# Performance work log

Measured on AMD Instinct MI355X. Metric: run time of the kernel, lower is better.

Reference implementation:

```python
import jax, jax.numpy as jnp
import numpy as np

N, T, D, H = 8192, 60, 6, 64  # stocks, lookback, d_feat, hidden_size
NEG_SLOPE = 0.01


def setup_inputs() -> dict:
    key = jax.random.key(0)
    ks = jax.random.split(key, 16)
    s = 0.1
    inp = {
        "x": jax.random.normal(ks[0], (N, D * T), jnp.float32),
        # GRU layer 0 (input D -> H), PyTorch gate order [r, z, n]
        "gru_Wih0": jax.random.normal(ks[1], (3 * H, D), jnp.float32) * s,
        "gru_Whh0": jax.random.normal(ks[2], (3 * H, H), jnp.float32) * s,
        "gru_bih0": jax.random.normal(ks[3], (3 * H,), jnp.float32) * s,
        "gru_bhh0": jax.random.normal(ks[4], (3 * H,), jnp.float32) * s,
        # GRU layer 1 (H -> H)
        "gru_Wih1": jax.random.normal(ks[5], (3 * H, H), jnp.float32) * s,
        "gru_Whh1": jax.random.normal(ks[6], (3 * H, H), jnp.float32) * s,
        "gru_bih1": jax.random.normal(ks[7], (3 * H,), jnp.float32) * s,
        "gru_bhh1": jax.random.normal(ks[8], (3 * H,), jnp.float32) * s,
        # attention head
        "transfer_W": jax.random.normal(ks[9], (H, H), jnp.float32) * s,
        "transfer_b": jax.random.normal(ks[10], (H,), jnp.float32) * s,
        "a": jax.random.normal(ks[11], (2 * H, 1), jnp.float32) * s,
        # output head
        "fc_W": jax.random.normal(ks[12], (H, H), jnp.float32) * s,
        "fc_b": jax.random.normal(ks[13], (H,), jnp.float32) * s,
        "out_W": jax.random.normal(ks[14], (1, H), jnp.float32) * s,
        "out_b": jax.random.normal(ks[15], (1,), jnp.float32) * s,
    }
    return inp


def _gru_layer(xs, Wih, Whh, bih, bhh):
    # xs: [T, N, in]; PyTorch GRU cell math, gate order r,z,n
    Hs = Whh.shape[1]

    def step(h, xt):
        gi = xt @ Wih.T + bih
        gh = h @ Whh.T + bhh
        ir, iz, inn = jnp.split(gi, 3, axis=-1)
        hr, hz, hn = jnp.split(gh, 3, axis=-1)
        r = jax.nn.sigmoid(ir + hr)
        z = jax.nn.sigmoid(iz + hz)
        n = jnp.tanh(inn + r * hn)
        h_new = (1.0 - z) * n + z * h
        return h_new, h_new

    h0 = jnp.zeros((xs.shape[1], Hs), xs.dtype)
    _, ys = jax.lax.scan(step, h0, xs)
    return ys  # [T, N, Hs]


def reference(x, gru_Wih0, gru_Whh0, gru_bih0, gru_bhh0,
              gru_Wih1, gru_Whh1, gru_bih1, gru_bhh1,
              transfer_W, transfer_b, a, fc_W, fc_b, out_W, out_b):
    # [N, D*T] -> [N, D, T] -> [T, N, D]
    xs = jnp.transpose(x.reshape(x.shape[0], D, -1), (2, 0, 1))
    ys0 = _gru_layer(xs, gru_Wih0, gru_Whh0, gru_bih0, gru_bhh0)
    ys1 = _gru_layer(ys0, gru_Wih1, gru_Whh1, gru_bih1, gru_bhh1)
    hidden = ys1[-1]  # [N, H] == out[:, -1, :]

    # self_attention: score[k, i] = a[:H].(W x_i) + a[H:].(W x_k)
    t = hidden @ transfer_W.T + transfer_b
    a1 = a[:H, 0]
    a2 = a[H:, 0]
    s1 = t @ a1  # contribution of column index i
    s2 = t @ a2  # contribution of row index k
    scores = jax.nn.leaky_relu(s2[:, None] + s1[None, :], NEG_SLOPE)  # [N, N]
    att = jax.nn.softmax(scores, axis=1)

    h = att @ hidden + hidden
    h = jax.nn.leaky_relu(h @ fc_W.T + fc_b, NEG_SLOPE)
    return (h @ out_W.T + out_b).squeeze()
```

## Files before the change

kernel.cpp:

```cpp
#include <hip/hip_runtime.h>
#include <hip/hip_bf16.h>
#include <math.h>

#define TSTEPS 60
#define DIN 6

typedef __attribute__((ext_vector_type(8))) short short8v;
typedef __attribute__((ext_vector_type(4))) float f32x4;
#define MFMA16 __builtin_amdgcn_mfma_f32_16x16x32_bf16

__device__ __forceinline__ float fast_rcp(float x) { return __builtin_amdgcn_rcpf(x); }
__device__ __forceinline__ float sigf(float x) { return fast_rcp(1.0f + __expf(-x)); }
__device__ __forceinline__ float tanhf_(float x) {
    return 1.0f - 2.0f * fast_rcp(__expf(2.0f * x) + 1.0f);
}
__device__ __forceinline__ unsigned short f2bf(float f) {
    unsigned u = __float_as_uint(f);
    u += 0x7fff + ((u >> 16) & 1);
    return (unsigned short)(u >> 16);
}
__device__ __forceinline__ float bf2f(unsigned short s) {
    return __uint_as_float(((unsigned)s) << 16);
}

__global__ __launch_bounds__(512, 1)
void gru_fused(const float* __restrict__ x,
               const float* __restrict__ Wih0, const float* __restrict__ Whh0,
               const float* __restrict__ bih0, const float* __restrict__ bhh0,
               const float* __restrict__ Wih1, const float* __restrict__ Whh1,
               const float* __restrict__ bih1, const float* __restrict__ bhh1,
               float* __restrict__ hidden)
{
    extern __shared__ char ldsb[];
    const int W0H = 0, W0L = 24576, W1IH = 49152, W1IL = 73728,
              W1HH = 98304, W1HL = 122880, HP = 147456;

    const int tid = threadIdx.x;
    const int l   = tid & 63;
    const int w   = tid >> 6;
    const int mt  = w >> 2;
    const int ur  = w & 3;
    const int l15 = l & 15;
    const int kb  = l >> 4;
    const int u_m = ur * 16 + l15;
    const int n0  = blockIdx.x * 32;

    for (int i = tid; i < 12288; i += 512) {
        int u = i >> 6, j = i & 63;
        int off = u * 128 + (((j >> 3) ^ (u & 7)) << 4) + (j & 7) * 2;
        float w0 = Whh0[i], w1 = Wih1[i], w2 = Whh1[i];
        unsigned short h0 = f2bf(w0); unsigned short l0 = f2bf(w0 - bf2f(h0));
        unsigned short h1 = f2bf(w1); unsigned short l1 = f2bf(w1 - bf2f(h1));
        unsigned short h2 = f2bf(w2); unsigned short l2 = f2bf(w2 - bf2f(h2));
        *(unsigned short*)(ldsb + W0H  + off) = h0;
        *(unsigned short*)(ldsb + W0L  + off) = l0;
        *(unsigned short*)(ldsb + W1IH + off) = h1;
        *(unsigned short*)(ldsb + W1IL + off) = l1;
        *(unsigned short*)(ldsb + W1HH + off) = h2;
        *(unsigned short*)(ldsb + W1HL + off) = l2;
    }
    for (int i = tid; i < 4096; i += 512) *(unsigned*)(ldsb + HP + i * 4) = 0u;

    float brz0_r = bih0[u_m] + bhh0[u_m];
    float brz0_z = bih0[64 + u_m] + bhh0[64 + u_m];
    float bi0n = bih0[128 + u_m], bh0n = bhh0[128 + u_m];
    float brz1_r = bih1[u_m] + bhh1[u_m];
    float brz1_z = bih1[64 + u_m] + bhh1[64 + u_m];
    float bi1n = bih1[128 + u_m], bh1n = bhh1[128 + u_m];

    float Wx[3][DIN];
#pragma unroll
    for (int g = 0; g < 3; ++g)
#pragma unroll
        for (int d = 0; d < DIN; ++d) Wx[g][d] = Wih0[(g * 64 + u_m) * DIN + d];

    const int rowA = mt * 16 + l15;
    const int bA0 = HP + rowA * 128 + ((kb ^ (rowA & 7)) << 4);
    const int bA1 = bA0 ^ 64;
    const int bB0 = u_m * 128 + ((kb ^ (u_m & 7)) << 4);
    const int bB1 = bB0 ^ 64;
    int wAo[4];
#pragma unroll
    for (int i = 0; i < 4; ++i) {
        int r = mt * 16 + kb * 4 + i;
        wAo[i] = HP + r * 128 + ((((u_m >> 3) & 7) ^ (r & 7)) << 4) + (u_m & 7) * 2;
    }
    const float* xp[4];
#pragma unroll
    for (int i = 0; i < 4; ++i)
        xp[i] = x + (size_t)(n0 + mt * 16 + kb * 4 + i) * (DIN * TSTEPS);

    float h0f[4] = {0.f, 0.f, 0.f, 0.f};
    float h1f[4] = {0.f, 0.f, 0.f, 0.f};

    __syncthreads();

#define LD8(o) (*(const short8v*)(ldsb + (o)))

    short8v B0[3][2][2];
#pragma unroll
    for (int g = 0; g < 3; ++g) {
        B0[g][0][0] = LD8(W0H + g * 8192 + bB0);
        B0[g][0][1] = LD8(W0H + g * 8192 + bB1);
        B0[g][1][0] = LD8(W0L + g * 8192 + bB0);
        B0[g][1][1] = LD8(W0L + g * 8192 + bB1);
    }

#pragma unroll 1
    for (int t = 0; t < TSTEPS; ++t) {
        float xv[4][DIN];
#pragma unroll
        for (int i = 0; i < 4; ++i)
#pragma unroll
            for (int d = 0; d < DIN; ++d) xv[i][d] = xp[i][d * TSTEPS + t];

        short8v aH0[2][2], aH1[2][2];
        aH0[0][0] = LD8(bA0);        aH0[1][0] = LD8(bA1);
        aH0[0][1] = LD8(bA0 + 4096); aH0[1][1] = LD8(bA1 + 4096);
        aH1[0][0] = LD8(bA0 + 8192); aH1[1][0] = LD8(bA1 + 8192);
        aH1[0][1] = LD8(bA0 + 12288); aH1[1][1] = LD8(bA1 + 12288);

        float gi0[4], gi1[4], gi2[4];
#pragma unroll
        for (int i = 0; i < 4; ++i) {
            float s0 = 0.f, s1 = 0.f, s2 = 0.f;
#pragma unroll
            for (int d = 0; d < DIN; ++d) {
                float xd = xv[i][d];
                s0 = fmaf(Wx[0][d], xd, s0);
                s1 = fmaf(Wx[1][d], xd, s1);
                s2 = fmaf(Wx[2][d], xd, s2);
            }
            gi0[i] = s0; gi1[i] = s1; gi2[i] = s2;
        }

        f32x4 Cr, Cz, Cnh;
#pragma unroll
        for (int i = 0; i < 4; ++i) {
            Cr[i] = brz0_r + gi0[i]; Cz[i] = brz0_z + gi1[i]; Cnh[i] = bh0n;
        }
        Cr = MFMA16(aH0[0][0], B0[0][0][0], Cr, 0, 0, 0);
        Cr = MFMA16(aH0[1][0], B0[0][0][1], Cr, 0, 0, 0);
        Cr = MFMA16(aH0[0][1], B0[0][0][0], Cr, 0, 0, 0);
        Cr = MFMA16(aH0[1][1], B0[0][0][1], Cr, 0, 0, 0);
        Cr = MFMA16(aH0[0][0], B0[0][1][0], Cr, 0, 0, 0);
        Cr = MFMA16(aH0[1][0], B0[0][1][1], Cr, 0, 0, 0);
        Cz = MFMA16(aH0[0][0], B0[1][0][0], Cz, 0, 0, 0);
        Cz = MFMA16(aH0[1][0], B0[1][0][1], Cz, 0, 0, 0);
        Cz = MFMA16(aH0[0][1], B0[1][0][0], Cz, 0, 0, 0);
        Cz = MFMA16(aH0[1][1], B0[1][0][1], Cz, 0, 0, 0);
        Cz = MFMA16(aH0[0][0], B0[1][1][0], Cz, 0, 0, 0);
        Cz = MFMA16(aH0[1][0], B0[1][1][1], Cz, 0, 0, 0);
        Cnh = MFMA16(aH0[0][0], B0[2][0][0], Cnh, 0, 0, 0);
        Cnh = MFMA16(aH0[1][0], B0[2][0][1], Cnh, 0, 0, 0);
        Cnh = MFMA16(aH0[0][1], B0[2][0][0], Cnh, 0, 0, 0);
        Cnh = MFMA16(aH0[1][1], B0[2][0][1], Cnh, 0, 0, 0);
        Cnh = MFMA16(aH0[0][0], B0[2][1][0], Cnh, 0, 0, 0);
        Cnh = MFMA16(aH0[1][0], B0[2][1][1], Cnh, 0, 0, 0);

        unsigned short hh[4], hl[4];
#pragma unroll
        for (int i = 0; i < 4; ++i) {
            float r = sigf(Cr[i]);
            float z = sigf(Cz[i]);
            float n = tanhf_(gi2[i] + bi0n + r * Cnh[i]);
            h0f[i] = (1.f - z) * n + z * h0f[i];
            hh[i] = f2bf(h0f[i]);
            hl[i] = f2bf(h0f[i] - bf2f(hh[i]));
        }
        __syncthreads();
#pragma unroll
        for (int i = 0; i < 4; ++i) {
            *(unsigned short*)(ldsb + wAo[i]) = hh[i];
            *(unsigned short*)(ldsb + wAo[i] + 4096) = hl[i];
        }
        __syncthreads();

        short8v aN[2][2];
        aN[0][0] = LD8(bA0);        aN[1][0] = LD8(bA1);
        aN[0][1] = LD8(bA0 + 4096); aN[1][1] = LD8(bA1 + 4096);

        f32x4 Dr, Dz, Dni, Dnh;
#pragma unroll
        for (int i = 0; i < 4; ++i) {
            Dr[i] = brz1_r; Dz[i] = brz1_z; Dni[i] = bi1n; Dnh[i] = bh1n;
        }
        {
            short8v bih_ = LD8(W1IH + bB0), bih1_ = LD8(W1IH + bB1);
            short8v bil_ = LD8(W1IL + bB0), bil1_ = LD8(W1IL + bB1);
            Dr = MFMA16(aN[0][0], bih_, Dr, 0, 0, 0);
            Dr = MFMA16(aN[1][0], bih1_, Dr, 0, 0, 0);
            Dr = MFMA16(aN[0][1], bih_, Dr, 0, 0, 0);
            Dr = MFMA16(aN[1][1], bih1_, Dr, 0, 0, 0);
            Dr = MFMA16(aN[0][0], bil_, Dr, 0, 0, 0);
            Dr = MFMA16(aN[1][0], bil1_, Dr, 0, 0, 0);
            short8v bhh_ = LD8(W1HH + bB0), bhh1_ = LD8(W1HH + bB1);
            short8v bhl_ = LD8(W1HL + bB0), bhl1_ = LD8(W1HL + bB1);
            Dr = MFMA16(aH1[0][0], bhh_, Dr, 0, 0, 0);
            Dr = MFMA16(aH1[1][0], bhh1_, Dr, 0, 0, 0);
            Dr = MFMA16(aH1[0][1], bhh_, Dr, 0, 0, 0);
            Dr = MFMA16(aH1[1][1], bhh1_, Dr, 0, 0, 0);
            Dr = MFMA16(aH1[0][0], bhl_, Dr, 0, 0, 0);
            Dr = MFMA16(aH1[1][0], bhl1_, Dr, 0, 0, 0);
        }
        {
            short8v bih_ = LD8(W1IH + 8192 + bB0), bih1_ = LD8(W1IH + 8192 + bB1);
            short8v bil_ = LD8(W1IL + 8192 + bB0), bil1_ = LD8(W1IL + 8192 + bB1);
            Dz = MFMA16(aN[0][0], bih_, Dz, 0, 0, 0);
            Dz = MFMA16(aN[1][0], bih1_, Dz, 0, 0, 0);
            Dz = MFMA16(aN[0][1], bih_, Dz, 0, 0, 0);
            Dz = MFMA16(aN[1][1], bih1_, Dz, 0, 0, 0);
            Dz = MFMA16(aN[0][0], bil_, Dz, 0, 0, 0);
            Dz = MFMA16(aN[1][0], bil1_, Dz, 0, 0, 0);
            short8v bhh_ = LD8(W1HH + 8192 + bB0), bhh1_ = LD8(W1HH + 8192 + bB1);
            short8v bhl_ = LD8(W1HL + 8192 + bB0), bhl1_ = LD8(W1HL + 8192 + bB1);
            Dz = MFMA16(aH1[0][0], bhh_, Dz, 0, 0, 0);
            Dz = MFMA16(aH1[1][0], bhh1_, Dz, 0, 0, 0);
            Dz = MFMA16(aH1[0][1], bhh_, Dz, 0, 0, 0);
            Dz = MFMA16(aH1[1][1], bhh1_, Dz, 0, 0, 0);
            Dz = MFMA16(aH1[0][0], bhl_, Dz, 0, 0, 0);
            Dz = MFMA16(aH1[1][0], bhl1_, Dz, 0, 0, 0);
        }
        {
            short8v bih_ = LD8(W1IH + 16384 + bB0), bih1_ = LD8(W1IH + 16384 + bB1);
            short8v bil_ = LD8(W1IL + 16384 + bB0), bil1_ = LD8(W1IL + 16384 + bB1);
            Dni = MFMA16(aN[0][0], bih_, Dni, 0, 0, 0);
            Dni = MFMA16(aN[1][0], bih1_, Dni, 0, 0, 0);
            Dni = MFMA16(aN[0][1], bih_, Dni, 0, 0, 0);
            Dni = MFMA16(aN[1][1], bih1_, Dni, 0, 0, 0);
            Dni = MFMA16(aN[0][0], bil_, Dni, 0, 0, 0);
            Dni = MFMA16(aN[1][0], bil1_, Dni, 0, 0, 0);
            short8v bhh_ = LD8(W1HH + 16384 + bB0), bhh1_ = LD8(W1HH + 16384 + bB1);
            short8v bhl_ = LD8(W1HL + 16384 + bB0), bhl1_ = LD8(W1HL + 16384 + bB1);
            Dnh = MFMA16(aH1[0][0], bhh_, Dnh, 0, 0, 0);
            Dnh = MFMA16(aH1[1][0], bhh1_, Dnh, 0, 0, 0);
            Dnh = MFMA16(aH1[0][1], bhh_, Dnh, 0, 0, 0);
            Dnh = MFMA16(aH1[1][1], bhh1_, Dnh, 0, 0, 0);
            Dnh = MFMA16(aH1[0][0], bhl_, Dnh, 0, 0, 0);
            Dnh = MFMA16(aH1[1][0], bhl1_, Dnh, 0, 0, 0);
        }
#pragma unroll
        for (int i = 0; i < 4; ++i) {
            float r = sigf(Dr[i]);
            float z = sigf(Dz[i]);
            float n = tanhf_(Dni[i] + r * Dnh[i]);
            h1f[i] = (1.f - z) * n + z * h1f[i];
            unsigned short hhi = f2bf(h1f[i]);
            *(unsigned short*)(ldsb + wAo[i] + 8192) = hhi;
            *(unsigned short*)(ldsb + wAo[i] + 12288) = f2bf(h1f[i] - bf2f(hhi));
        }
        __syncthreads();
    }

#pragma unroll
    for (int i = 0; i < 4; ++i)
        hidden[(size_t)(n0 + mt * 16 + kb * 4 + i) * 64 + u_m] = h1f[i];
#undef LD8
}

__global__ __launch_bounds__(256)
void transposeH(const float* __restrict__ hidden, float* __restrict__ hiddenT)
{
    __shared__ float tile[64][65];
    int b = blockIdx.x, tid = threadIdx.x;
    for (int i = tid; i < 4096; i += 256) {
        int r = i >> 6, c = i & 63;
        tile[c][r] = hidden[(size_t)(b * 64 + r) * 64 + c];
    }
    __syncthreads();
    for (int i = tid; i < 4096; i += 256) {
        int c = i >> 6, r = i & 63;
        hiddenT[(size_t)c * 8192 + b * 64 + r] = tile[c][r];
    }
}

__global__ __launch_bounds__(256)
void attn_prep(const float* __restrict__ hidden, const float* __restrict__ tW,
               const float* __restrict__ tb, const float* __restrict__ a,
               float* __restrict__ s1, float* __restrict__ s2)
{
    __shared__ float WT[64 * 64];
    __shared__ float hrow[4][64];
    int tid = threadIdx.x, c = tid & 63, rw = tid >> 6;
    for (int i = tid; i < 4096; i += 256) WT[i] = tW[(i & 63) * 64 + (i >> 6)];
    int row = blockIdx.x * 4 + rw;
    hrow[rw][c] = hidden[(size_t)row * 64 + c];
    __syncthreads();
    float tc = tb[c];
    for (int u = 0; u < 64; ++u) tc += WT[u * 64 + c] * hrow[rw][u];
    float p1 = tc * a[c], p2 = tc * a[64 + c];
#pragma unroll
    for (int o = 32; o; o >>= 1) { p1 += __shfl_xor(p1, o); p2 += __shfl_xor(p2, o); }
    if (c == 0) { s1[row] = p1; s2[row] = p2; }
}

__global__ __launch_bounds__(1024)
void sort_s1(const float* __restrict__ s1, float* __restrict__ s1s, int* __restrict__ perm)
{
    extern __shared__ float smem[];
    float* key = smem;
    int*   idx = (int*)(smem + 8192);
    int tid = threadIdx.x;
    for (int i = tid; i < 8192; i += 1024) { key[i] = s1[i]; idx[i] = i; }
    __syncthreads();
    for (int sz = 2; sz <= 8192; sz <<= 1) {
        for (int stride = sz >> 1; stride > 0; stride >>= 1) {
            for (int p = tid; p < 4096; p += 1024) {
                int low = p & (stride - 1);
                int i = ((p - low) << 1) + low;
                int j = i + stride;
                bool asc = (i & sz) == 0;
                float ki = key[i], kj = key[j];
                bool sw = asc ? (ki > kj) : (ki < kj);
                if (sw) {
                    key[i] = kj; key[j] = ki;
                    int tmp = idx[i]; idx[i] = idx[j]; idx[j] = tmp;
                }
            }
            __syncthreads();
        }
    }
    for (int i = tid; i < 8192; i += 1024) { s1s[i] = key[i]; perm[i] = idx[i]; }
}

__global__ __launch_bounds__(64)
void scans(const float* __restrict__ s1s, const int* __restrict__ perm,
           const float* __restrict__ hiddenT,
           float* __restrict__ SufE, float* __restrict__ SufEH,
           float* __restrict__ PreE, float* __restrict__ PreEH)
{
    int lane = threadIdx.x;
    int b = blockIdx.x;
    int c = b % 65;
    bool neg = b >= 65;
    const float* hT = hiddenT + (size_t)(c < 64 ? c : 0) * 8192;
    if (!neg) {
        if (lane == 0) { if (c < 64) SufEH[8192 * 64 + c] = 0.f; else SufE[8192] = 0.f; }
        float carry = 0.f;
        for (int ch = 127; ch >= 0; --ch) {
            int k = ch * 64 + lane;
            float e = expf(s1s[k]);
            float v = (c < 64) ? e * hT[perm[k]] : e;
#pragma unroll
            for (int o = 1; o < 64; o <<= 1) {
                float tv = __shfl_down(v, o);
                if (lane + o < 64) v += tv;
            }
            v += carry;
            if (c < 64) SufEH[(size_t)k * 64 + c] = v; else SufE[k] = v;
            carry = __shfl(v, 0);
        }
    } else {
        float carry = 0.f;
        for (int ch = 0; ch < 128; ++ch) {
            int k = ch * 64 + lane;
            float e = expf(0.01f * s1s[k]);
            float term = (c < 64) ? e * hT[perm[k]] : e;
            float v = term;
#pragma unroll
            for (int o = 1; o < 64; o <<= 1) {
                float tv = __shfl_up(v, o);
                if (lane >= o) v += tv;
            }
            float excl = v - term + carry;
            if (c < 64) PreEH[(size_t)k * 64 + c] = excl; else PreE[k] = excl;
            carry += __shfl(v, 63);
        }
        if (lane == 0) { if (c < 64) PreEH[8192 * 64 + c] = carry; else PreE[8192] = carry; }
    }
}

__global__ __launch_bounds__(256)
void finalize(const float* __restrict__ hidden, const float* __restrict__ s1s,
              const float* __restrict__ s2v,
              const float* __restrict__ SufE, const float* __restrict__ SufEH,
              const float* __restrict__ PreE, const float* __restrict__ PreEH,
              const float* __restrict__ fcW, const float* __restrict__ fcb,
              const float* __restrict__ outW, const float* __restrict__ outb,
              float* __restrict__ out)
{
    __shared__ float fcWT[64 * 64];
    __shared__ float h2[4][64];
    int tid = threadIdx.x, c = tid & 63, rw = tid >> 6;
    for (int i = tid; i < 4096; i += 256) fcWT[i] = fcW[(i & 63) * 64 + (i >> 6)];
    int row = blockIdx.x * 4 + rw;
    float s2 = s2v[row];
    float th = -s2;
    int lo = 0, hi = 8192;
    while (lo < hi) { int mid = (lo + hi) >> 1; if (s1s[mid] > th) hi = mid; else lo = mid + 1; }
    int k = lo;
    float ep = expf(s2);
    float en = expf(0.01f * s2);
    float den = ep * SufE[k] + en * PreE[k];
    float num = ep * SufEH[(size_t)k * 64 + c] + en * PreEH[(size_t)k * 64 + c];
    h2[rw][c] = num / den + hidden[(size_t)row * 64 + c];
    __syncthreads();
    float y = fcb[c];
    for (int u = 0; u < 64; ++u) y += fcWT[u * 64 + c] * h2[rw][u];
    y = y > 0.f ? y : 0.01f * y;
    float o = y * outW[c];
#pragma unroll
    for (int s = 32; s; s >>= 1) o += __shfl_xor(o, s);
    if (c == 0) out[row] = o + outb[0];
}

extern "C" void kernel_launch(void* const* d_in, const int* in_sizes, int n_in,
                              void* d_out, int out_size, void* d_ws, size_t ws_size,
                              hipStream_t stream)
{
    const float* x     = (const float*)d_in[0];
    const float* Wih0  = (const float*)d_in[1];
    const float* Whh0  = (const float*)d_in[2];
    const float* bih0  = (const float*)d_in[3];
    const float* bhh0  = (const float*)d_in[4];
    const float* Wih1  = (const float*)d_in[5];
    const float* Whh1  = (const float*)d_in[6];
    const float* bih1  = (const float*)d_in[7];
    const float* bhh1  = (const float*)d_in[8];
    const float* tW    = (const float*)d_in[9];
    const float* tb    = (const float*)d_in[10];
    const float* a     = (const float*)d_in[11];
    const float* fcW   = (const float*)d_in[12];
    const float* fcb   = (const float*)d_in[13];
    const float* outW  = (const float*)d_in[14];
    const float* outb  = (const float*)d_in[15];

    float* ws      = (float*)d_ws;
    float* hidden  = ws;
    float* s1      = hidden + 8192 * 64;
    float* s2      = s1 + 8192;
    float* s1s     = s2 + 8192;
    int*   perm    = (int*)(s1s + 8192);
    float* SufE    = (float*)(perm + 8192);
    float* PreE    = SufE + 8200;
    float* SufEH   = PreE + 8200;
    float* PreEH   = SufEH + 8193 * 64;
    float* hiddenT = PreEH + 8193 * 64;

    hipStreamCaptureStatus cap = hipStreamCaptureStatusNone;
    hipStreamIsCapturing(stream, &cap);
    if (cap == hipStreamCaptureStatusNone) {
        hipFuncSetAttribute(reinterpret_cast<const void*>(gru_fused),
                            hipFuncAttributeMaxDynamicSharedMemorySize, 163840);
        hipFuncSetAttribute(reinterpret_cast<const void*>(sort_s1),
                            hipFuncAttributeMaxDynamicSharedMemorySize, 65536);
    }

    gru_fused<<<256, 512, 163840, stream>>>(x, Wih0, Whh0, bih0, bhh0,
                                            Wih1, Whh1, bih1, bhh1, hidden);
    transposeH<<<128, 256, 0, stream>>>(hidden, hiddenT);
    attn_prep<<<2048, 256, 0, stream>>>(hidden, tW, tb, a, s1, s2);
    sort_s1<<<1, 1024, 65536, stream>>>(s1, s1s, perm);
    scans<<<130, 64, 0, stream>>>(s1s, perm, hiddenT, SufE, SufEH, PreE, PreEH);
    finalize<<<2048, 256, 0, stream>>>(hidden, s1s, s2, SufE, SufEH, PreE, PreEH,
                                       fcW, fcb, outW, outb, (float*)d_out);
}
```

Baseline: 483.3 us.

## Replace sort-and-scan attention with dense bf16-split MFMA attention kernel

Drops the single-block bitonic sort, the sequential prefix/suffix scans and the binary-search finalize. In their place, a dense N×N attention kernel builds the factorised exp weights (exp of the positive or the 0.01-scaled branch, chosen per pair) and multiplies them against a transposed hidden matrix on bf16 MFMA. Each operand is split into high and low bf16 parts, using three MFMAs per tile to keep accuracy near fp32. The exp terms are precomputed in attn_prep, and the fc head becomes a separate kernel. This removes serial, latency-bound sort and scan stages but does quadratic work instead of N log N, and it reads the transposed hidden matrix repeatedly from cache.

```diff
diff --git a/kernel.cpp b/kernel.cpp
--- a/kernel.cpp
+++ b/kernel.cpp
@@ -259,25 +259,11 @@
 }
 
 __global__ __launch_bounds__(256)
-void transposeH(const float* __restrict__ hidden, float* __restrict__ hiddenT)
-{
-    __shared__ float tile[64][65];
-    int b = blockIdx.x, tid = threadIdx.x;
-    for (int i = tid; i < 4096; i += 256) {
-        int r = i >> 6, c = i & 63;
-        tile[c][r] = hidden[(size_t)(b * 64 + r) * 64 + c];
-    }
-    __syncthreads();
-    for (int i = tid; i < 4096; i += 256) {
-        int c = i >> 6, r = i & 63;
-        hiddenT[(size_t)c * 8192 + b * 64 + r] = tile[c][r];
-    }
-}
-
-__global__ __launch_bounds__(256)
 void attn_prep(const float* __restrict__ hidden, const float* __restrict__ tW,
                const float* __restrict__ tb, const float* __restrict__ a,
-               float* __restrict__ s1, float* __restrict__ s2)
+               float* __restrict__ s1, float* __restrict__ s2,
+               float* __restrict__ E1p, float* __restrict__ E1n,
+               float* __restrict__ E2p, float* __restrict__ E2n)
 {
     __shared__ float WT[64 * 64];
     __shared__ float hrow[4][64];
@@ -291,112 +277,154 @@
     float p1 = tc * a[c], p2 = tc * a[64 + c];
 #pragma unroll
     for (int o = 32; o; o >>= 1) { p1 += __shfl_xor(p1, o); p2 += __shfl_xor(p2, o); }
-    if (c == 0) { s1[row] = p1; s2[row] = p2; }
-}
-
-__global__ __launch_bounds__(1024)
-void sort_s1(const float* __restrict__ s1, float* __restrict__ s1s, int* __restrict__ perm)
-{
-    extern __shared__ float smem[];
-    float* key = smem;
-    int*   idx = (int*)(smem + 8192);
-    int tid = threadIdx.x;
-    for (int i = tid; i < 8192; i += 1024) { key[i] = s1[i]; idx[i] = i; }
+    if (c == 0) {
+        s1[row] = p1; s2[row] = p2;
+        E1p[row] = expf(p1); E1n[row] = expf(0.01f * p1);
+        E2p[row] = expf(p2); E2n[row] = expf(0.01f * p2);
+    }
+}
+
+__global__ __launch_bounds__(256)
+void transposeHbf(const float* __restrict__ hidden,
+                  unsigned short* __restrict__ hiTh, unsigned short* __restrict__ hiTl)
+{
+    __shared__ float tile[64][65];
+    int b = blockIdx.x, tid = threadIdx.x;
+    for (int i = tid; i < 4096; i += 256) {
+        int r = i >> 6, c = i & 63;
+        tile[c][r] = hidden[(size_t)(b * 64 + r) * 64 + c];
+    }
     __syncthreads();
-    for (int sz = 2; sz <= 8192; sz <<= 1) {
-        for (int stride = sz >> 1; stride > 0; stride >>= 1) {
-            for (int p = tid; p < 4096; p += 1024) {
-                int low = p & (stride - 1);
-                int i = ((p - low) << 1) + low;
-                int j = i + stride;
-                bool asc = (i & sz) == 0;
-                float ki = key[i], kj = key[j];
-                bool sw = asc ? (ki > kj) : (ki < kj);
-                if (sw) {
-                    key[i] = kj; key[j] = ki;
-                    int tmp = idx[i]; idx[i] = idx[j]; idx[j] = tmp;
-                }
+    int c = tid & 63, seg = tid >> 6;
+    unsigned short oh[16], ol[16];
+#pragma unroll
+    for (int k = 0; k < 16; ++k) {
+        float v = tile[c][seg * 16 + k];
+        unsigned short h = f2bf(v);
+        oh[k] = h; ol[k] = f2bf(v - bf2f(h));
+    }
+    size_t base = (size_t)c * 8192 + b * 64 + seg * 16;
+    *(short8v*)(hiTh + base)     = *(const short8v*)(oh);
+    *(short8v*)(hiTh + base + 8) = *(const short8v*)(oh + 8);
+    *(short8v*)(hiTl + base)     = *(const short8v*)(ol);
+    *(short8v*)(hiTl + base + 8) = *(const short8v*)(ol + 8);
+}
+
+__global__ __launch_bounds__(256)
+void flash_attn(const float* __restrict__ s1, const float* __restrict__ s2,
+                const float* __restrict__ E1p, const float* __restrict__ E1n,
+                const float* __restrict__ E2p, const float* __restrict__ E2n,
+                const unsigned short* __restrict__ hiTh,
+                const unsigned short* __restrict__ hiTl,
+                const float* __restrict__ hidden, float* __restrict__ h2)
+{
+    __shared__ float comb[4][64][17];
+    const int tid = threadIdx.x;
+    const int l = tid & 63, w = tid >> 6;
+    const int iw = w >> 1, jh = w & 1;
+    const int l15 = l & 15, kb = l >> 4;
+    const int i0 = blockIdx.x * 32 + iw * 16;
+
+    const float s2i  = s2[i0 + l15];
+    const float E2pv = E2p[i0 + l15];
+    const float E2nv = E2n[i0 + l15];
+
+    f32x4 C[4];
+#pragma unroll
+    for (int ct = 0; ct < 4; ++ct)
+#pragma unroll
+        for (int r = 0; r < 4; ++r) C[ct][r] = 0.f;
+    float den = 0.f;
+
+#pragma unroll 2
+    for (int it = 0; it < 128; ++it) {
+        const int jk = jh * 4096 + it * 32 + kb * 8;
+        float4 s1a = *(const float4*)(s1 + jk);
+        float4 s1b = *(const float4*)(s1 + jk + 4);
+        float4 p1a = *(const float4*)(E1p + jk);
+        float4 p1b = *(const float4*)(E1p + jk + 4);
+        float4 n1a = *(const float4*)(E1n + jk);
+        float4 n1b = *(const float4*)(E1n + jk + 4);
+
+        short8v Bh[4], Bl[4];
+#pragma unroll
+        for (int ct = 0; ct < 4; ++ct) {
+            size_t off = (size_t)(ct * 16 + l15) * 8192 + jk;
+            Bh[ct] = *(const short8v*)(hiTh + off);
+            Bl[ct] = *(const short8v*)(hiTl + off);
+        }
+
+        unsigned short ah[8], al[8];
+#define MK(e, sv, pv, nv)                                            \
+        {                                                            \
+            float s = s2i + (sv);                                    \
+            bool cpos = s > 0.f;                                     \
+            float w1 = cpos ? (pv) : (nv);                           \
+            float w2 = cpos ? E2pv : E2nv;                           \
+            float ev = w1 * w2;                                      \
+            den += ev;                                               \
+            unsigned short hx = f2bf(ev);                            \
+            ah[e] = hx; al[e] = f2bf(ev - bf2f(hx));                 \
+        }
+        MK(0, s1a.x, p1a.x, n1a.x) MK(1, s1a.y, p1a.y, n1a.y)
+        MK(2, s1a.z, p1a.z, n1a.z) MK(3, s1a.w, p1a.w, n1a.w)
+        MK(4, s1b.x, p1b.x, n1b.x) MK(5, s1b.y, p1b.y, n1b.y)
+        MK(6, s1b.z, p1b.z, n1b.z) MK(7, s1b.w, p1b.w, n1b.w)
+#undef MK
+        short8v Ah = { (short)ah[0], (short)ah[1], (short)ah[2], (short)ah[3],
+                       (short)ah[4], (short)ah[5], (short)ah[6], (short)ah[7] };
+        short8v Al = { (short)al[0], (short)al[1], (short)al[2], (short)al[3],
+                       (short)al[4], (short)al[5], (short)al[6], (short)al[7] };
+
+#pragma unroll
+        for (int ct = 0; ct < 4; ++ct) {
+            C[ct] = MFMA16(Ah, Bh[ct], C[ct], 0, 0, 0);
+            C[ct] = MFMA16(Al, Bh[ct], C[ct], 0, 0, 0);
+            C[ct] = MFMA16(Ah, Bl[ct], C[ct], 0, 0, 0);
+        }
+    }
+
+    den += __shfl_xor(den, 16);
+    den += __shfl_xor(den, 32);
+
+#pragma unroll
+    for (int ct = 0; ct < 4; ++ct)
+#pragma unroll
+        for (int r = 0; r < 4; ++r) comb[w][l][ct * 4 + r] = C[ct][r];
+    comb[w][l][16] = den;
+    __syncthreads();
+
+    if (jh == 0) {
+        float den_t = comb[w][l][16] + comb[w + 1][l][16];
+#pragma unroll
+        for (int ct = 0; ct < 4; ++ct) {
+#pragma unroll
+            for (int r = 0; r < 4; ++r) {
+                int rr = kb * 4 + r;
+                float num = comb[w][l][ct * 4 + r] + comb[w + 1][l][ct * 4 + r];
+                float dv = __shfl(den_t, rr);
+                size_t oidx = (size_t)(i0 + rr) * 64 + ct * 16 + l15;
+                h2[oidx] = num / dv + hidden[oidx];
             }
-            __syncthreads();
-        }
-    }
-    for (int i = tid; i < 8192; i += 1024) { s1s[i] = key[i]; perm[i] = idx[i]; }
-}
-
-__global__ __launch_bounds__(64)
-void scans(const float* __restrict__ s1s, const int* __restrict__ perm,
-           const float* __restrict__ hiddenT,
-           float* __restrict__ SufE, float* __restrict__ SufEH,
-           float* __restrict__ PreE, float* __restrict__ PreEH)
-{
-    int lane = threadIdx.x;
-    int b = blockIdx.x;
-    int c = b % 65;
-    bool neg = b >= 65;
-    const float* hT = hiddenT + (size_t)(c < 64 ? c : 0) * 8192;
-    if (!neg) {
-        if (lane == 0) { if (c < 64) SufEH[8192 * 64 + c] = 0.f; else SufE[8192] = 0.f; }
-        float carry = 0.f;
-        for (int ch = 127; ch >= 0; --ch) {
-            int k = ch * 64 + lane;
-            float e = expf(s1s[k]);
-            float v = (c < 64) ? e * hT[perm[k]] : e;
-#pragma unroll
-            for (int o = 1; o < 64; o <<= 1) {
-                float tv = __shfl_down(v, o);
-                if (lane + o < 64) v += tv;
-            }
-            v += carry;
-            if (c < 64) SufEH[(size_t)k * 64 + c] = v; else SufE[k] = v;
-            carry = __shfl(v, 0);
-        }
-    } else {
-        float carry = 0.f;
-        for (int ch = 0; ch < 128; ++ch) {
-            int k = ch * 64 + lane;
-            float e = expf(0.01f * s1s[k]);
-            float term = (c < 64) ? e * hT[perm[k]] : e;
-            float v = term;
-#pragma unroll
-            for (int o = 1; o < 64; o <<= 1) {
-                float tv = __shfl_up(v, o);
-                if (lane >= o) v += tv;
-            }
-            float excl = v - term + carry;
-            if (c < 64) PreEH[(size_t)k * 64 + c] = excl; else PreE[k] = excl;
-            carry += __shfl(v, 63);
-        }
-        if (lane == 0) { if (c < 64) PreEH[8192 * 64 + c] = carry; else PreE[8192] = carry; }
+        }
     }
 }
 
 __global__ __launch_bounds__(256)
-void finalize(const float* __restrict__ hidden, const float* __restrict__ s1s,
-              const float* __restrict__ s2v,
-              const float* __restrict__ SufE, const float* __restrict__ SufEH,
-              const float* __restrict__ PreE, const float* __restrict__ PreEH,
-              const float* __restrict__ fcW, const float* __restrict__ fcb,
-              const float* __restrict__ outW, const float* __restrict__ outb,
-              float* __restrict__ out)
+void fc_out(const float* __restrict__ h2,
+            const float* __restrict__ fcW, const float* __restrict__ fcb,
+            const float* __restrict__ outW, const float* __restrict__ outb,
+            float* __restrict__ out)
 {
     __shared__ float fcWT[64 * 64];
-    __shared__ float h2[4][64];
+    __shared__ float hrow[4][64];
     int tid = threadIdx.x, c = tid & 63, rw = tid >> 6;
     for (int i = tid; i < 4096; i += 256) fcWT[i] = fcW[(i & 63) * 64 + (i >> 6)];
     int row = blockIdx.x * 4 + rw;
-    float s2 = s2v[row];
-    float th = -s2;
-    int lo = 0, hi = 8192;
-    while (lo < hi) { int mid = (lo + hi) >> 1; if (s1s[mid] > th) hi = mid; else lo = mid + 1; }
-    int k = lo;
-    float ep = expf(s2);
-    float en = expf(0.01f * s2);
-    float den = ep * SufE[k] + en * PreE[k];
-    float num = ep * SufEH[(size_t)k * 64 + c] + en * PreEH[(size_t)k * 64 + c];
-    h2[rw][c] = num / den + hidden[(size_t)row * 64 + c];
+    hrow[rw][c] = h2[(size_t)row * 64 + c];
     __syncthreads();
     float y = fcb[c];
-    for (int u = 0; u < 64; ++u) y += fcWT[u * 64 + c] * h2[rw][u];
+    for (int u = 0; u < 64; ++u) y += fcWT[u * 64 + c] * hrow[rw][u];
     y = y > 0.f ? y : 0.01f * y;
     float o = y * outW[c];
 #pragma unroll
@@ -427,31 +455,29 @@
 
     float* ws      = (float*)d_ws;
     float* hidden  = ws;
-    float* s1      = hidden + 8192 * 64;
+    float* s1      = hidden + 524288;
     float* s2      = s1 + 8192;
-    float* s1s     = s2 + 8192;
-    int*   perm    = (int*)(s1s + 8192);
-    float* SufE    = (float*)(perm + 8192);
-    float* PreE    = SufE + 8200;
-    float* SufEH   = PreE + 8200;
-    float* PreEH   = SufEH + 8193 * 64;
-    float* hiddenT = PreEH + 8193 * 64;
+    float* E1p     = s2 + 8192;
+    float* E1n     = E1p + 8192;
+    float* E2p     = E1n + 8192;
+    float* E2n     = E2p + 8192;
+    unsigned short* hiTh = (unsigned short*)(ws + 573440);
+    unsigned short* hiTl = hiTh + 524288;
+    float* h2      = ws + 573440 + 524288;
 
     hipStreamCaptureStatus cap = hipStreamCaptureStatusNone;
     hipStreamIsCapturing(stream, &cap);
     if (cap == hipStreamCaptureStatusNone) {
         hipFuncSetAttribute(reinterpret_cast<const void*>(gru_fused),
                             hipFuncAttributeMaxDynamicSharedMemorySize, 163840);
-        hipFuncSetAttribute(reinterpret_cast<const void*>(sort_s1),
-                            hipFuncAttributeMaxDynamicSharedMemorySize, 65536);
     }
 
     gru_fused<<<256, 512, 163840, stream>>>(x, Wih0, Whh0, bih0, bhh0,
                                             Wih1, Whh1, bih1, bhh1, hidden);
-    transposeH<<<128, 256, 0, stream>>>(hidden, hiddenT);
-    attn_prep<<<2048, 256, 0, stream>>>(hidden, tW, tb, a, s1, s2);
-    sort_s1<<<1, 1024, 65536, stream>>>(s1, s1s, perm);
-    scans<<<130, 64, 0, stream>>>(s1s, perm, hiddenT, SufE, SufEH, PreE, PreEH);
-    finalize<<<2048, 256, 0, stream>>>(hidden, s1s, s2, SufE, SufEH, PreE, PreEH,
-                                       fcW, fcb, outW, outb, (float*)d_out);
-}
+    attn_prep<<<2048, 256, 0, stream>>>(hidden, tW, tb, a, s1, s2,
+                                        E1p, E1n, E2p, E2n);
+    transposeHbf<<<128, 256, 0, stream>>>(hidden, hiTh, hiTl);
+    flash_attn<<<256, 256, 0, stream>>>(s1, s2, E1p, E1n, E2p, E2n,
+                                        hiTh, hiTl, hidden, h2);
+    fc_out<<<2048, 256, 0, stream>>>(h2, fcW, fcb, outW, outb, (float*)d_out);
+}
```

New measurement: 433.1 us. -10.4%, faster.
